# Kernel tuning notes

Measured on AMD Instinct MI355X. Metric: run time of the kernel, lower is better.

Reference implementation:

```python
import jax, jax.numpy as jnp
import numpy as np


def setup_inputs() -> dict:
    key = jax.random.key(0)
    k0, k1, k2, k3 = jax.random.split(key, 4)
    B, S, D, F, E = 2, 2048, 1024, 4096, 8
    scale = 0.02
    return {
        "x": jax.random.normal(k0, (B, S, D), jnp.float32),
        "gate_w": jax.random.normal(k1, (E, D), jnp.float32) * scale,
        "gate_b": jnp.zeros((E,), jnp.float32),
        "w1": jax.random.normal(k2, (E, D, F), jnp.float32) * scale,
        "b1": jnp.zeros((E, F), jnp.float32),
        "w2": jax.random.normal(k3, (E, F, D), jnp.float32) * scale,
        "b2": jnp.zeros((E, D), jnp.float32),
        "top_k": 2,
    }


def reference(x, gate_w, gate_b, w1, b1, w2, b2, top_k):
    B, S, D = x.shape
    E = gate_w.shape[0]
    xt = x.reshape(-1, D)                                   # [T, D]
    T = xt.shape[0]

    # Router: softmax over gate logits, then top-k and renormalize.
    gate_probs = jax.nn.softmax(xt @ gate_w.T + gate_b, axis=-1)   # [T, E]
    weights, selected = jax.lax.top_k(gate_probs, top_k)           # [T, k]
    weights = weights / jnp.sum(weights, axis=-1, keepdims=True)

    # Per-token combine weights over experts (zero where not selected),
    # equivalent to the per-expert gather/scatter loop in the original.
    combine = jnp.zeros((T, E), x.dtype).at[
        jnp.arange(T)[:, None], selected
    ].add(weights)                                                 # [T, E]

    # Expert MLPs (dense over experts, masked combine).
    h = jax.nn.silu(jnp.einsum("td,edf->etf", xt, w1) + b1[:, None, :])  # [E, T, F]
    expert_out = jnp.einsum("etf,efd->etd", h, w2) + b2[:, None, :]      # [E, T, D]
    out = jnp.einsum("etd,te->td", expert_out, combine)                  # [T, D]
    return out.reshape(B, S, D)
```

## Files before the change

kernel.cpp:

```cpp
#include <hip/hip_runtime.h>

#define T_TOK 4096
#define DIM   1024
#define FDIM  4096
#define NEXP  8

typedef __bf16 bf16x8 __attribute__((ext_vector_type(8)));
typedef __bf16 bf16x4 __attribute__((ext_vector_type(4)));
typedef float  f32x4  __attribute__((ext_vector_type(4)));

__device__ __forceinline__ void glds16(const void* g, void* l) {
    __builtin_amdgcn_global_load_lds(
        (const __attribute__((address_space(1))) void*)g,
        (__attribute__((address_space(3))) void*)l, 16, 0, 0);
}

__global__ __launch_bounds__(64)
void moe_router(const float* __restrict__ x,
                const float* __restrict__ gw,
                const float* __restrict__ gb,
                const int*   __restrict__ topk_p,
                int*   __restrict__ counts,
                int*   __restrict__ bucket,
                float* __restrict__ bweight,
                __bf16* __restrict__ xb) {
    const int t = blockIdx.x;
    const int lane = threadIdx.x;
    float part[NEXP];
#pragma unroll
    for (int e = 0; e < NEXP; ++e) part[e] = 0.f;
    const float* xrow = x + (size_t)t * DIM;
    __bf16* xbrow = xb + (size_t)t * DIM;
#pragma unroll
    for (int r = 0; r < 4; ++r) {
        int c = r * 256 + lane * 4;
        float4 v = *(const float4*)&xrow[c];
        bf16x4 o; o[0]=(__bf16)v.x; o[1]=(__bf16)v.y; o[2]=(__bf16)v.z; o[3]=(__bf16)v.w;
        *(bf16x4*)&xbrow[c] = o;
#pragma unroll
        for (int e = 0; e < NEXP; ++e) {
            float4 g = *(const float4*)&gw[e * DIM + c];
            part[e] += v.x*g.x + v.y*g.y + v.z*g.z + v.w*g.w;
        }
    }
#pragma unroll
    for (int off = 32; off > 0; off >>= 1) {
#pragma unroll
        for (int e = 0; e < NEXP; ++e) part[e] += __shfl_xor(part[e], off);
    }
    if (lane == 0) {
        int k = topk_p[0];
        if (k < 1) k = 1;
        if (k > NEXP) k = NEXP;
        float p[NEXP];
        float mx = -1e30f;
#pragma unroll
        for (int e = 0; e < NEXP; ++e) {
            p[e] = part[e] + gb[e];
            mx = fmaxf(mx, p[e]);
        }
#pragma unroll
        for (int e = 0; e < NEXP; ++e) p[e] = __expf(p[e] - mx);
        bool used[NEXP];
#pragma unroll
        for (int e = 0; e < NEXP; ++e) used[e] = false;
        int sel[NEXP]; float selp[NEXP]; float wsum = 0.f;
        for (int j = 0; j < k; ++j) {
            int best = 0; float bv = -1.f;
            for (int e = 0; e < NEXP; ++e)
                if (!used[e] && p[e] > bv) { bv = p[e]; best = e; }
            used[best] = true; sel[j] = best; selp[j] = bv; wsum += bv;
        }
        for (int j = 0; j < k; ++j) {
            int e = sel[j];
            int pos = atomicAdd(&counts[e], 1);
            bucket[e * T_TOK + pos]  = t;
            bweight[e * T_TOK + pos] = selp[j] / wsum;
        }
    }
}

__global__ __launch_bounds__(256)
void transpose_cvt(const float* __restrict__ in, __bf16* __restrict__ out,
                   int R, int C) {
    const size_t zo = (size_t)blockIdx.z * R * C;
    in += zo; out += zo;
    __shared__ float ts[64][65];
    const int c0 = blockIdx.x * 64, r0 = blockIdx.y * 64;
    const int t = threadIdx.x;
    const int rr = t >> 2, cc4 = (t & 3) * 16;
    const float* src = in + (size_t)(r0 + rr) * C + c0 + cc4;
#pragma unroll
    for (int i = 0; i < 4; ++i) {
        float4 v = *(const float4*)(src + i * 4);
        ts[rr][cc4 + i*4 + 0] = v.x; ts[rr][cc4 + i*4 + 1] = v.y;
        ts[rr][cc4 + i*4 + 2] = v.z; ts[rr][cc4 + i*4 + 3] = v.w;
    }
    __syncthreads();
    const int oc = rr, orc = cc4;
    bf16x8 o0, o1;
#pragma unroll
    for (int i = 0; i < 8; ++i) o0[i] = (__bf16)ts[orc + i][oc];
#pragma unroll
    for (int i = 0; i < 8; ++i) o1[i] = (__bf16)ts[orc + 8 + i][oc];
    __bf16* dst = out + (size_t)(c0 + oc) * R + r0 + orc;
    *(bf16x8*)dst = o0;
    *(bf16x8*)(dst + 8) = o1;
}

__global__ __launch_bounds__(64)
void build_work(const int* __restrict__ counts, int* __restrict__ hdr) {
    __shared__ int off1[NEXP + 1];
    const int lane = threadIdx.x;
    if (lane == 0) {
        int a = 0;
        for (int e = 0; e < NEXP; ++e) {
            off1[e] = a;
            a += (counts[e] + 127) >> 7;
        }
        off1[NEXP] = a;
        hdr[0] = a;
    }
    __syncthreads();
    for (int e = 0; e < NEXP; ++e) {
        int n1 = off1[e + 1] - off1[e];
        for (int j = lane; j < n1; j += 64) hdr[8 + off1[e] + j] = (e << 16) | j;
    }
}


__global__ __launch_bounds__(256, 3)
void moe_gemm1(const __bf16* __restrict__ xb,
               const __bf16* __restrict__ w1t,
               const float*  __restrict__ b1,
               const int*    __restrict__ counts,
               const int*    __restrict__ bucket,
               const int*    __restrict__ hdr,
               __bf16* __restrict__ H) {
    __shared__ __bf16 smem[16384];
    __shared__ int tok_s[128];
    const int tid = threadIdx.x;
    const int wave = tid >> 6, lane = tid & 63;
    const int wm = wave & 1, wn = wave >> 1;
    const int quad = lane >> 4, l15 = lane & 15;
    const int lrow = lane >> 2;
    const int lk8  = (lane & 3) * 8;
    char* sb = (char*)smem;
    char* dA0 = sb + wave * 2048;
    char* dA1 = sb + 8192 + wave * 2048;
    char* dB0 = sb + 16384 + wave * 2048;
    char* dB1 = sb + 24576 + wave * 2048;

    const int n1 = hdr[0];
    const int total = n1 * (FDIM / 128);
    for (int u = blockIdx.x; u < total; u += gridDim.x) {
        const int entry = hdr[8 + (u % n1)];
        const int e = entry >> 16, tile = entry & 0xffff;
        const int nb = (u / n1) * 128;
        const int cnt = counts[e];
        if (tid < 128) {
            int r = tile * 128 + tid;
            if (r >= cnt) r = cnt - 1;
            tok_s[tid] = bucket[e * T_TOK + r];
        }
        __syncthreads();

        const int ar0 = wave * 32 + lrow;
        const __bf16* pA0 = xb + (size_t)tok_s[ar0]      * DIM + lk8;
        const __bf16* pA1 = xb + (size_t)tok_s[ar0 + 16] * DIM + lk8;
        const __bf16* pB0 = w1t + ((size_t)e * FDIM + nb + wave * 32 + lrow) * DIM + lk8;
        const __bf16* pB1 = pB0 + (size_t)16 * DIM;

        f32x4 acc[4][4];
#pragma unroll
        for (int i = 0; i < 4; ++i)
#pragma unroll
            for (int j = 0; j < 4; ++j) acc[i][j] = (f32x4){0.f,0.f,0.f,0.f};

        for (int k0 = 0; k0 < DIM; k0 += 64) {
            glds16(pA0 + k0,      dA0);
            glds16(pA0 + k0 + 32, dA1);
            glds16(pA1 + k0,      dA0 + 1024);
            glds16(pA1 + k0 + 32, dA1 + 1024);
            glds16(pB0 + k0,      dB0);
            glds16(pB0 + k0 + 32, dB1);
            glds16(pB1 + k0,      dB0 + 1024);
            glds16(pB1 + k0 + 32, dB1 + 1024);
            __syncthreads();
#pragma unroll
            for (int kk = 0; kk < 2; ++kk) {
                bf16x8 af[4], bfr[4];
#pragma unroll
                for (int i = 0; i < 4; ++i)
                    af[i] = *(const bf16x8*)&smem[kk*4096 + (wm*64 + i*16 + l15)*32 + quad*8];
#pragma unroll
                for (int j = 0; j < 4; ++j)
                    bfr[j] = *(const bf16x8*)&smem[8192 + kk*4096 + (wn*64 + j*16 + l15)*32 + quad*8];
#pragma unroll
                for (int i = 0; i < 4; ++i)
#pragma unroll
                    for (int j = 0; j < 4; ++j)
                        acc[i][j] = __builtin_amdgcn_mfma_f32_16x16x32_bf16(
                            af[i], bfr[j], acc[i][j], 0, 0, 0);
            }
            __syncthreads();
        }

        __bf16* stg = (__bf16*)(sb + wave * 2304);
        const float* b1e = b1 + e * FDIM + nb + wn * 64;
#pragma unroll
        for (int i = 0; i < 4; ++i) {
#pragma unroll
            for (int j = 0; j < 4; ++j) {
                float bias = b1e[j * 16 + l15];
#pragma unroll
                for (int r = 0; r < 4; ++r) {
                    float v = acc[i][j][r] + bias;
                    float s = v / (1.f + __expf(-v));
                    stg[(quad*4 + r) * 72 + j*16 + l15] = (__bf16)s;
                }
            }
            int prow = tile * 128 + wm * 64 + i * 16 + lrow;
            if (prow < cnt) {
                bf16x8 v0 = *(const bf16x8*)&stg[lrow * 72 + (lane & 3) * 16];
                bf16x8 v1 = *(const bf16x8*)&stg[lrow * 72 + (lane & 3) * 16 + 8];
                __bf16* dst = H + (size_t)(e * T_TOK + prow) * FDIM
                              + nb + wn * 64 + (lane & 3) * 16;
                *(bf16x8*)dst = v0;
                *(bf16x8*)(dst + 8) = v1;
            }
        }
        __syncthreads();
    }
}

__global__ __launch_bounds__(256, 3)
void moe_gemm2(const __bf16* __restrict__ H,
               const __bf16* __restrict__ w2t,
               const float*  __restrict__ b2,
               const int*    __restrict__ counts,
               const int*    __restrict__ bucket,
               const float*  __restrict__ bweight,
               const int*    __restrict__ hdr,
               float* __restrict__ out) {
    __shared__ __bf16 smem[16384];
    __shared__ int   tok_s[128];
    __shared__ float w_s[128];
    const int tid = threadIdx.x;
    const int wave = tid >> 6, lane = tid & 63;
    const int wm = wave & 1, wn = wave >> 1;
    const int quad = lane >> 4, l15 = lane & 15;
    const int lrow = lane >> 2;
    const int lk8  = (lane & 3) * 8;
    char* sb = (char*)smem;
    char* dA0 = sb + wave * 2048;
    char* dA1 = sb + 8192 + wave * 2048;
    char* dB0 = sb + 16384 + wave * 2048;
    char* dB1 = sb + 24576 + wave * 2048;

    const int n1 = hdr[0];
    const int total = n1 * (DIM / 128);
    for (int u = blockIdx.x; u < total; u += gridDim.x) {
        const int entry = hdr[8 + (u % n1)];
        const int e = entry >> 16, tile = entry & 0xffff;
        const int nb = (u / n1) * 128;
        const int cnt = counts[e];
        if (tid < 128) {
            int r  = tile * 128 + tid;
            int rc = r < cnt ? r : cnt - 1;
            tok_s[tid] = bucket[e * T_TOK + rc];
            w_s[tid]   = bweight[e * T_TOK + rc];
        }
        __syncthreads();

        const __bf16* pA0 = H + (size_t)(e * T_TOK + tile * 128 + wave * 32 + lrow) * FDIM + lk8;
        const __bf16* pA1 = pA0 + (size_t)16 * FDIM;
        const __bf16* pB0 = w2t + ((size_t)e * DIM + nb + wave * 32 + lrow) * FDIM + lk8;
        const __bf16* pB1 = pB0 + (size_t)16 * FDIM;

        f32x4 acc[4][4];
#pragma unroll
        for (int i = 0; i < 4; ++i)
#pragma unroll
            for (int j = 0; j < 4; ++j) acc[i][j] = (f32x4){0.f,0.f,0.f,0.f};

        for (int k0 = 0; k0 < FDIM; k0 += 64) {
            glds16(pA0 + k0,      dA0);
            glds16(pA0 + k0 + 32, dA1);
            glds16(pA1 + k0,      dA0 + 1024);
            glds16(pA1 + k0 + 32, dA1 + 1024);
            glds16(pB0 + k0,      dB0);
            glds16(pB0 + k0 + 32, dB1);
            glds16(pB1 + k0,      dB0 + 1024);
            glds16(pB1 + k0 + 32, dB1 + 1024);
            __syncthreads();
#pragma unroll
            for (int kk = 0; kk < 2; ++kk) {
                bf16x8 af[4], bfr[4];
#pragma unroll
                for (int i = 0; i < 4; ++i)
                    af[i] = *(const bf16x8*)&smem[kk*4096 + (wm*64 + i*16 + l15)*32 + quad*8];
#pragma unroll
                for (int j = 0; j < 4; ++j)
                    bfr[j] = *(const bf16x8*)&smem[8192 + kk*4096 + (wn*64 + j*16 + l15)*32 + quad*8];
#pragma unroll
                for (int i = 0; i < 4; ++i)
#pragma unroll
                    for (int j = 0; j < 4; ++j)
                        acc[i][j] = __builtin_amdgcn_mfma_f32_16x16x32_bf16(
                            af[i], bfr[j], acc[i][j], 0, 0, 0);
            }
            __syncthreads();
        }

#pragma unroll
        for (int i = 0; i < 4; ++i)
#pragma unroll
            for (int j = 0; j < 4; ++j)
#pragma unroll
                for (int r = 0; r < 4; ++r) {
                    int m = wm*64 + i*16 + quad*4 + r;
                    int prow = tile * 128 + m;
                    if (prow < cnt) {
                        int dc = nb + wn*64 + j*16 + l15;
                        float v = acc[i][j][r] + b2[e * DIM + dc];
                        atomicAdd(&out[(size_t)tok_s[m] * DIM + dc], w_s[m] * v);
                    }
                }
        __syncthreads();
    }
}

extern "C" void kernel_launch(void* const* d_in, const int* in_sizes, int n_in,
                              void* d_out, int out_size, void* d_ws, size_t ws_size,
                              hipStream_t stream) {
    const float* x  = (const float*)d_in[0];
    const float* gw = (const float*)d_in[1];
    const float* gb = (const float*)d_in[2];
    const float* w1 = (const float*)d_in[3];
    const float* b1 = (const float*)d_in[4];
    const float* w2 = (const float*)d_in[5];
    const float* b2 = (const float*)d_in[6];
    const int* topk = (const int*)d_in[7];
    float* out = (float*)d_out;

    char* ws = (char*)d_ws;
    size_t off = 0;
    int* counts = (int*)(ws + off);    off += 256;
    int* bucket = (int*)(ws + off);    off += (size_t)NEXP * T_TOK * 4;
    float* bw   = (float*)(ws + off);  off += (size_t)NEXP * T_TOK * 4;
    int* hdr    = (int*)(ws + off);    off += 4096;
    off = (off + 255) & ~(size_t)255;
    __bf16* xb  = (__bf16*)(ws + off); off += (size_t)T_TOK * DIM * 2;
    __bf16* w1t = (__bf16*)(ws + off); off += (size_t)NEXP * DIM * FDIM * 2;
    __bf16* w2t = (__bf16*)(ws + off); off += (size_t)NEXP * FDIM * DIM * 2;
    __bf16* H   = (__bf16*)(ws + off);

    hipMemsetAsync(counts, 0, 256, stream);
    hipMemsetAsync(out, 0, (size_t)out_size * 4, stream);

    moe_router<<<T_TOK, 64, 0, stream>>>(x, gw, gb, topk, counts, bucket, bw, xb);
    transpose_cvt<<<dim3(FDIM/64, DIM/64, NEXP), 256, 0, stream>>>(w1, w1t, DIM, FDIM);
    transpose_cvt<<<dim3(DIM/64, FDIM/64, NEXP), 256, 0, stream>>>(w2, w2t, FDIM, DIM);
    build_work<<<1, 64, 0, stream>>>(counts, hdr);

    moe_gemm1<<<1024, 256, 0, stream>>>(xb, w1t, b1, counts, bucket, hdr, H);
    moe_gemm2<<<512, 256, 0, stream>>>(H, w2t, b2, counts, bucket, bw, hdr, out);
}
```

Baseline: 820.6 us.

## Split-K the second expert GEMM, add XCD-aware tile swizzle, raise occupancy

The second expert GEMM is split along the F dimension into two halves, with partial sums accumulated into the output by the existing atomics and the bias added only by the first half. This doubles the number of work tiles, so more blocks can run at once on the small tile count. Tile indices are remapped so consecutive logical tiles land on the same XCD, aiming for better L2 reuse of the shared weight and activation tiles. Launch bounds move to 4 blocks per CU and both grids are doubled. The cost is twice the atomic output traffic in the second GEMM and possible register pressure from the tighter launch bound.

```diff
diff --git a/kernel.cpp b/kernel.cpp
--- a/kernel.cpp
+++ b/kernel.cpp
@@ -13,6 +13,12 @@
     __builtin_amdgcn_global_load_lds(
         (const __attribute__((address_space(1))) void*)g,
         (__attribute__((address_space(3))) void*)l, 16, 0, 0);
+}
+
+__device__ __forceinline__ int xcd_swz(int phys, int total) {
+    int q = total >> 3, r = total & 7;
+    int x = phys & 7, i = phys >> 3;
+    return (x < r ? x * (q + 1) : r * (q + 1) + (x - r) * q) + i;
 }
 
 __global__ __launch_bounds__(64)
@@ -129,7 +135,7 @@
 }
 
 
-__global__ __launch_bounds__(256, 3)
+__global__ __launch_bounds__(256, 4)
 void moe_gemm1(const __bf16* __restrict__ xb,
                const __bf16* __restrict__ w1t,
                const float*  __restrict__ b1,
@@ -153,7 +159,8 @@
 
     const int n1 = hdr[0];
     const int total = n1 * (FDIM / 128);
-    for (int u = blockIdx.x; u < total; u += gridDim.x) {
+    for (int phys = blockIdx.x; phys < total; phys += gridDim.x) {
+        const int u = xcd_swz(phys, total);
         const int entry = hdr[8 + (u % n1)];
         const int e = entry >> 16, tile = entry & 0xffff;
         const int nb = (u / n1) * 128;
@@ -234,7 +241,10 @@
     }
 }
 
-__global__ __launch_bounds__(256, 3)
+#define KSPLIT 2
+#define KHALF  (FDIM / KSPLIT)
+
+__global__ __launch_bounds__(256, 4)
 void moe_gemm2(const __bf16* __restrict__ H,
                const __bf16* __restrict__ w2t,
                const float*  __restrict__ b2,
@@ -259,11 +269,14 @@
     char* dB1 = sb + 24576 + wave * 2048;
 
     const int n1 = hdr[0];
-    const int total = n1 * (DIM / 128);
-    for (int u = blockIdx.x; u < total; u += gridDim.x) {
+    const int total = n1 * (DIM / 128) * KSPLIT;
+    for (int phys = blockIdx.x; phys < total; phys += gridDim.x) {
+        const int u = xcd_swz(phys, total);
         const int entry = hdr[8 + (u % n1)];
         const int e = entry >> 16, tile = entry & 0xffff;
-        const int nb = (u / n1) * 128;
+        const int rest = u / n1;
+        const int nb = (rest & 7) * 128;
+        const int kc = rest >> 3;
         const int cnt = counts[e];
         if (tid < 128) {
             int r  = tile * 128 + tid;
@@ -273,9 +286,12 @@
         }
         __syncthreads();
 
-        const __bf16* pA0 = H + (size_t)(e * T_TOK + tile * 128 + wave * 32 + lrow) * FDIM + lk8;
+        const size_t kbase = (size_t)kc * KHALF;
+        const __bf16* pA0 = H + (size_t)(e * T_TOK + tile * 128 + wave * 32 + lrow) * FDIM
+                              + kbase + lk8;
         const __bf16* pA1 = pA0 + (size_t)16 * FDIM;
-        const __bf16* pB0 = w2t + ((size_t)e * DIM + nb + wave * 32 + lrow) * FDIM + lk8;
+        const __bf16* pB0 = w2t + ((size_t)e * DIM + nb + wave * 32 + lrow) * FDIM
+                              + kbase + lk8;
         const __bf16* pB1 = pB0 + (size_t)16 * FDIM;
 
         f32x4 acc[4][4];
@@ -284,7 +300,7 @@
 #pragma unroll
             for (int j = 0; j < 4; ++j) acc[i][j] = (f32x4){0.f,0.f,0.f,0.f};
 
-        for (int k0 = 0; k0 < FDIM; k0 += 64) {
+        for (int k0 = 0; k0 < KHALF; k0 += 64) {
             glds16(pA0 + k0,      dA0);
             glds16(pA0 + k0 + 32, dA1);
             glds16(pA1 + k0,      dA0 + 1024);
@@ -323,7 +339,7 @@
                     int prow = tile * 128 + m;
                     if (prow < cnt) {
                         int dc = nb + wn*64 + j*16 + l15;
-                        float v = acc[i][j][r] + b2[e * DIM + dc];
+                        float v = acc[i][j][r] + (kc == 0 ? b2[e * DIM + dc] : 0.f);
                         atomicAdd(&out[(size_t)tok_s[m] * DIM + dc], w_s[m] * v);
                     }
                 }
@@ -364,6 +380,6 @@
     transpose_cvt<<<dim3(DIM/64, FDIM/64, NEXP), 256, 0, stream>>>(w2, w2t, FDIM, DIM);
     build_work<<<1, 64, 0, stream>>>(counts, hdr);
 
-    moe_gemm1<<<1024, 256, 0, stream>>>(xb, w1t, b1, counts, bucket, hdr, H);
-    moe_gemm2<<<512, 256, 0, stream>>>(H, w2t, b2, counts, bucket, bw, hdr, out);
-}
+    moe_gemm1<<<2048, 256, 0, stream>>>(xb, w1t, b1, counts, bucket, hdr, H);
+    moe_gemm2<<<1024, 256, 0, stream>>>(H, w2t, b2, counts, bucket, bw, hdr, out);
+}
```

After: 725.7 us. 11.6% less time.
